# Optimization experiments

Measured on AMD Instinct MI355X. Metric: run time of the kernel, lower is better.

The kernel has to match this reference:

```python
import jax, jax.numpy as jnp
import numpy as np

DIM = 1024
HEADS = 16
HIDDEN = 4 * DIM

def _gelu_erf(x):
    # GELU via erf, matching the torch module exactly
    return x * 0.5 * (1.0 + jax.lax.erf(x / jnp.sqrt(2.0).astype(x.dtype)))

def setup_inputs() -> dict:
    key = jax.random.key(0)
    ks = jax.random.split(key, 12)
    s = 0.02
    x = jax.random.normal(ks[0], (2, 2048, DIM), dtype=jnp.float32)
    # MHSA params
    ln1_g = jnp.ones((DIM,), jnp.float32)
    ln1_b = jnp.zeros((DIM,), jnp.float32)
    w_qkv = jax.random.normal(ks[1], (DIM, 3 * DIM), jnp.float32) * s  # no bias
    w_proj = jax.random.normal(ks[2], (DIM, DIM), jnp.float32) * s
    b_proj = jnp.zeros((DIM,), jnp.float32)
    # ResMLP params
    ln2_g = jnp.ones((DIM,), jnp.float32)
    ln2_b = jnp.zeros((DIM,), jnp.float32)
    w1 = jax.random.normal(ks[3], (DIM, HIDDEN), jnp.float32) * s
    b1 = jnp.zeros((HIDDEN,), jnp.float32)
    w2 = jax.random.normal(ks[4], (HIDDEN, DIM), jnp.float32) * s
    b2 = jnp.zeros((DIM,), jnp.float32)
    return {"x": x, "ln1_g": ln1_g, "ln1_b": ln1_b, "w_qkv": w_qkv,
            "w_proj": w_proj, "b_proj": b_proj, "ln2_g": ln2_g, "ln2_b": ln2_b,
            "w1": w1, "b1": b1, "w2": w2, "b2": b2}

def _layernorm(x, g, b, eps=1e-5):
    mu = jnp.mean(x, axis=-1, keepdims=True)
    var = jnp.mean(jnp.square(x - mu), axis=-1, keepdims=True)
    return (x - mu) * jax.lax.rsqrt(var + eps) * g + b

def reference(x, ln1_g, ln1_b, w_qkv, w_proj, b_proj, ln2_g, ln2_b, w1, b1, w2, b2):
    B, N, C = x.shape
    H = HEADS
    hd = C // H
    scale = hd ** -0.5
    # --- MHSA (dropout is identity in eval) ---
    h = _layernorm(x, ln1_g, ln1_b)
    qkv = (h @ w_qkv).reshape(B, N, 3, H, hd)
    q = jnp.transpose(qkv[:, :, 0], (0, 2, 1, 3))  # [B,H,N,hd]
    k = jnp.transpose(qkv[:, :, 1], (0, 2, 1, 3))
    v = jnp.transpose(qkv[:, :, 2], (0, 2, 1, 3))
    attn = jax.nn.softmax(jnp.einsum('bhnd,bhmd->bhnm', q, k) * scale, axis=-1)
    out = jnp.einsum('bhnm,bhmd->bhnd', attn, v)
    out = jnp.transpose(out, (0, 2, 1, 3)).reshape(B, N, C)
    x = x + out @ w_proj + b_proj
    # --- ResMLP ---
    h = _layernorm(x, ln2_g, ln2_b)
    h = _gelu_erf(h @ w1 + b1)
    x = x + h @ w2 + b2
    return x
```

## Files before the change

kernel.cpp:

```cpp
#include <hip/hip_runtime.h>
#include <stdint.h>


#define DIMC 1024
#define HIDN 4096
#define SEQ  2048
#define TOK  4096

typedef __bf16 bf16x8 __attribute__((ext_vector_type(8)));
typedef float  f32x4  __attribute__((ext_vector_type(4)));
typedef unsigned short ushort8 __attribute__((ext_vector_type(8)));

__device__ inline unsigned short f2bf(float f) {
  union { float f; unsigned u; } v; v.f = f;
  unsigned u = v.u;
  return (unsigned short)((u + 0x7fffu + ((u >> 16) & 1u)) >> 16);
}

__device__ inline unsigned cvt_pk_bf16(float a, float b) {
  unsigned r;
  asm("v_cvt_pk_bf16_f32 %0, %1, %2" : "=v"(r) : "v"(a), "v"(b));
  return r;
}

#if __has_builtin(__builtin_amdgcn_exp2f)
__device__ inline float fast_exp2(float x) { return __builtin_amdgcn_exp2f(x); }
#else
__device__ inline float fast_exp2(float x) { return exp2f(x); }
#endif

__device__ inline f32x4 mfma_bf16(bf16x8 a, bf16x8 b, f32x4 c) {
  return __builtin_amdgcn_mfma_f32_16x16x32_bf16(a, b, c, 0, 0, 0);
}

typedef const __attribute__((address_space(1))) unsigned int* as1_u32p;
typedef __attribute__((address_space(3))) unsigned int* as3_u32p;
__device__ inline void gload_lds16(const unsigned short* g, unsigned short* l) {
  __builtin_amdgcn_global_load_lds((as1_u32p)(const void*)g, (as3_u32p)(void*)l,
                                   16, 0, 0);
}

__global__ __launch_bounds__(256)
void transpose_cast4(const float* __restrict__ wa, unsigned short* __restrict__ ta,
                     const float* __restrict__ wb, unsigned short* __restrict__ tb,
                     const float* __restrict__ wc, unsigned short* __restrict__ tc,
                     const float* __restrict__ wd, unsigned short* __restrict__ td) {
  __shared__ float tile[32][33];
  const int bid = blockIdx.x;
  const float* w; unsigned short* wt; int K, N, bx, by;
  if (bid < 3072)      { w = wa; wt = ta; K = 1024; N = 3072; bx = bid % 96;  by = bid / 96; }
  else if (bid < 4096) { int i = bid - 3072; w = wb; wt = tb; K = 1024; N = 1024; bx = i % 32;  by = i / 32; }
  else if (bid < 8192) { int i = bid - 4096; w = wc; wt = tc; K = 1024; N = 4096; bx = i % 128; by = i / 128; }
  else                 { int i = bid - 8192; w = wd; wt = td; K = 4096; N = 1024; bx = i % 32;  by = i / 32; }
  const int k0 = by * 32;
  const int n0 = bx * 32;
  const int tx = threadIdx.x & 31;
  const int ty = threadIdx.x >> 5;
#pragma unroll
  for (int i = 0; i < 4; i++)
    tile[ty + i * 8][tx] = w[(size_t)(k0 + ty + i * 8) * N + n0 + tx];
  __syncthreads();
#pragma unroll
  for (int i = 0; i < 4; i++)
    wt[(size_t)(n0 + ty + i * 8) * K + k0 + tx] = f2bf(tile[tx][ty + i * 8]);
}

__global__ __launch_bounds__(256)
void ln_kernel(const float* __restrict__ x, const float* __restrict__ g,
               const float* __restrict__ b, unsigned short* __restrict__ out) {
  const int row = blockIdx.x;
  const int tid = threadIdx.x;
  const float4* xr = (const float4*)&x[(size_t)row * DIMC];
  float4 v = xr[tid];
  float s  = v.x + v.y + v.z + v.w;
  float sq = v.x * v.x + v.y * v.y + v.z * v.z + v.w * v.w;
#pragma unroll
  for (int off = 32; off > 0; off >>= 1) {
    s  += __shfl_xor(s, off, 64);
    sq += __shfl_xor(sq, off, 64);
  }
  __shared__ float red[8];
  if ((tid & 63) == 0) { red[tid >> 6] = s; red[4 + (tid >> 6)] = sq; }
  __syncthreads();
  s  = red[0] + red[1] + red[2] + red[3];
  sq = red[4] + red[5] + red[6] + red[7];
  const float mu  = s * (1.0f / DIMC);
  const float var = sq * (1.0f / DIMC) - mu * mu;
  const float rs  = rsqrtf(var + 1e-5f);
  const int c = tid * 4;
  float vv[4] = {v.x, v.y, v.z, v.w};
#pragma unroll
  for (int j = 0; j < 4; j++)
    out[(size_t)row * DIMC + c + j] = f2bf((vv[j] - mu) * rs * g[c + j] + b[c + j]);
}

template <int EPI, int TN>
__global__ __launch_bounds__(256, (TN == 64) ? 4 : 3)
void gemm_bt(const unsigned short* __restrict__ A,
             const unsigned short* __restrict__ Bt,
             float* __restrict__ Cf, unsigned short* __restrict__ Cb,
             const float* __restrict__ bias, const float* __restrict__ res,
             int M, int N, int K,
             unsigned short* __restrict__ qd,
             unsigned short* __restrict__ kTd,
             unsigned short* __restrict__ vd) {
  constexpr int NU = TN / 32;
  constexpr int BP = TN / 32;
  __shared__ unsigned short As[128 * 64];
  __shared__ unsigned short Bs[TN * 64];
  const int gx  = N / TN;
  const int bid = blockIdx.x;
  const int xcd = bid & 7;
  const int lin = bid >> 3;
  const int bx  = lin % gx;
  const int by  = (xcd << 2) + lin / gx;
  const int tid  = threadIdx.x;
  const int lane = tid & 63;
  const int wave = tid >> 6;
  const int m0 = by * 128;
  const int n0 = bx * TN;
  const int wm = (wave >> 1) * 64;
  const int wn = (wave & 1) * (TN / 2);
  const int lm = lane & 15;
  const int lg = lane >> 4;
  const int r8 = tid >> 3;
  const int c8 = tid & 7;
  const int csrc = ((c8 ^ (r8 & 7)) * 8);

  const unsigned short* gA = &A [(size_t)(m0 + r8) * K + csrc];
  const unsigned short* gB = &Bt[(size_t)(n0 + r8) * K + csrc];

  f32x4 acc[4][NU];
#pragma unroll
  for (int t = 0; t < 4; t++)
#pragma unroll
    for (int u = 0; u < NU; u++) acc[t][u] = {0.f, 0.f, 0.f, 0.f};

  const int x0 = (lg ^ (lm & 7)) * 8;
  const int x1 = ((4 + lg) ^ (lm & 7)) * 8;

  for (int k0 = 0; k0 < K; k0 += 64) {
    __syncthreads();
#pragma unroll
    for (int p = 0; p < 4; p++)
      gload_lds16(gA + (size_t)p * 32 * K + k0, &As[p * 2048 + wave * 512]);
#pragma unroll
    for (int p = 0; p < BP; p++)
      gload_lds16(gB + (size_t)p * 32 * K + k0, &Bs[p * 2048 + wave * 512]);
    __syncthreads();
#pragma unroll
    for (int sub = 0; sub < 2; sub++) {
      const int xo = sub ? x1 : x0;
      bf16x8 af[4], bfr[NU];
#pragma unroll
      for (int t = 0; t < 4; t++)  af[t]  = *(const bf16x8*)&As[(wm + t * 16 + lm) * 64 + xo];
#pragma unroll
      for (int u = 0; u < NU; u++) bfr[u] = *(const bf16x8*)&Bs[(wn + u * 16 + lm) * 64 + xo];
#pragma unroll
      for (int t = 0; t < 4; t++)
#pragma unroll
        for (int u = 0; u < NU; u++)
          acc[t][u] = mfma_bf16(af[t], bfr[u], acc[t][u]);
    }
  }

#pragma unroll
  for (int t = 0; t < 4; t++) {
    const int row = m0 + wm + t * 16 + lg * 4;
#pragma unroll
    for (int u = 0; u < NU; u++) {
      const int col = n0 + wn + u * 16 + lm;
#pragma unroll
      for (int r = 0; r < 4; r++) {
        float v = acc[t][u][r];
        size_t idx = (size_t)(row + r) * N + col;
        if (EPI == 0) {
          const int rr = row + r;
          const int bb = rr >> 11, key = rr & (SEQ - 1);
          if (col < 1024) {
            qd[(size_t)rr * 1024 + col] = f2bf(v * 0.18033688011112042f);
          } else if (col < 2048) {
            const int d = col - 1024, h = d >> 6, dd = d & 63;
            kTd[(((size_t)(bb * 16 + h)) * SEQ + key) * 64 + dd] = f2bf(v);
          } else {
            vd[(size_t)rr * 1024 + (col - 2048)] = f2bf(v);
          }
        } else if (EPI == 1) {
          Cf[idx] = v + bias[col] + res[idx];
        } else {
          float xg = v + bias[col];
          Cb[idx] = f2bf(0.5f * xg * (1.0f + erff(xg * 0.70710678118654752f)));
        }
      }
    }
  }
}

__global__ __launch_bounds__(256)
void v_transpose(const unsigned short* __restrict__ vd,
                 unsigned short* __restrict__ vT) {
  const int kt = blockIdx.x;
  const int bh = blockIdx.y;
  const int b = bh >> 4, h = bh & 15;
  const int tid = threadIdx.x;
  __shared__ unsigned short tile[64 * 72];
  const int tok = tid >> 2;
  const int ch  = tid & 3;
  const size_t srow = (size_t)(b * SEQ + kt * 64 + tok) * 1024 + h * 64;
  ushort8 va = *(const ushort8*)&vd[srow + ch * 8];
  ushort8 vb = *(const ushort8*)&vd[srow + 32 + ch * 8];
  *(ushort8*)&tile[tok * 72 + ch * 8] = va;
  *(ushort8*)&tile[tok * 72 + 32 + ch * 8] = vb;
  __syncthreads();
  const int d = tid >> 2;
  ushort8 o0, o1;
#pragma unroll
  for (int j = 0; j < 8; j++) {
    o0[j] = tile[(ch * 8 + j) * 72 + d];
    o1[j] = tile[((ch + 4) * 8 + j) * 72 + d];
  }
  const size_t vdst = ((size_t)bh * 64 + d) * SEQ + kt * 64;
  *(ushort8*)&vT[vdst + ch * 8] = o0;
  *(ushort8*)&vT[vdst + 32 + ch * 8] = o1;
}

__global__ __launch_bounds__(256, 2)
void attn_kernel(const unsigned short* __restrict__ qbuf,
                 const unsigned short* __restrict__ kT,
                 const unsigned short* __restrict__ vT,
                 unsigned short* __restrict__ out) {
  const int bid = blockIdx.x;
  const int xcd = bid & 7;
  const int lin = bid >> 3;
  const int bh  = (xcd << 2) + (lin >> 4);
  const int qt  = lin & 15;
  const int b  = bh >> 4;
  const int h  = bh & 15;
  const int tid  = threadIdx.x;
  const int lane = tid & 63;
  const int wave = tid >> 6;
  const int ks   = wave >> 1;
  const int qh   = wave & 1;
  const int lm = lane & 15;
  const int lg = lane >> 4;

  __shared__ f32x4 shbuf[4096];
  unsigned short* Ks = (unsigned short*)shbuf;
  unsigned short* Vs = (unsigned short*)shbuf + 8192;
  unsigned short* Ps = (unsigned short*)shbuf + 16384;

  const int qrow_base = b * SEQ + qt * 128 + qh * 64;
  bf16x8 qb[4][2];
#pragma unroll
  for (int s = 0; s < 4; s++)
#pragma unroll
    for (int c = 0; c < 2; c++)
      qb[s][c] = *(const bf16x8*)&qbuf[(size_t)(qrow_base + s * 16 + lm) * 1024 +
                                       h * 64 + c * 32 + lg * 8];

  f32x4 o[4][4];
#pragma unroll
  for (int dt = 0; dt < 4; dt++)
#pragma unroll
    for (int s = 0; s < 4; s++) o[dt][s] = {0.f, 0.f, 0.f, 0.f};
  float li[4] = {0.f, 0.f, 0.f, 0.f};

  const unsigned short* kbp = &kT[(size_t)bh * SEQ * 64];
  const unsigned short* vbp = &vT[(size_t)bh * 64 * SEQ];
  const int ts   = tid & 127;
  const int srow = ts >> 3;
  const int slog = ((ts & 7) ^ (srow & 7)) * 8;
  const int koff = ks * 1024;
  const int xk0 = ((lg)     ^ (lm & 7)) * 8;
  const int xk1 = ((4 + lg) ^ (lm & 7)) * 8;
  unsigned short* ksb = Ks + ks * 4096;
  unsigned short* vsb = Vs + ks * 4096;
  unsigned short* psb = Ps + wave * 4096;
  unsigned short* kdst = ksb + ((ts >> 6) * 512);
  unsigned short* vdst = vsb + ((ts >> 6) * 512);

  for (int kt = 0; kt < 16; kt++) {
    __syncthreads();
#pragma unroll
    for (int p = 0; p < 4; p++) {
      gload_lds16(&kbp[(size_t)(koff + kt * 64 + p * 16 + srow) * 64 + slog],
                  kdst + p * 1024);
      gload_lds16(&vbp[(size_t)(p * 16 + srow) * SEQ + koff + kt * 64 + slog],
                  vdst + p * 1024);
    }
    __syncthreads();

#pragma unroll
    for (int u = 0; u < 4; u++) {
      bf16x8 ka0 = *(const bf16x8*)&ksb[(u * 16 + lm) * 64 + xk0];
      bf16x8 ka1 = *(const bf16x8*)&ksb[(u * 16 + lm) * 64 + xk1];
      f32x4 st[4];
#pragma unroll
      for (int s = 0; s < 4; s++) {
        f32x4 z = {0.f, 0.f, 0.f, 0.f};
        z = mfma_bf16(ka0, qb[s][0], z);
        z = mfma_bf16(ka1, qb[s][1], z);
        st[s] = z;
      }
#pragma unroll
      for (int s = 0; s < 4; s++) {
        float p0 = fast_exp2(st[s][0] - 8.0f);
        float p1 = fast_exp2(st[s][1] - 8.0f);
        float p2 = fast_exp2(st[s][2] - 8.0f);
        float p3 = fast_exp2(st[s][3] - 8.0f);
        li[s] += (p0 + p1) + (p2 + p3);
        uint2 pk;
        pk.x = cvt_pk_bf16(p0, p1);
        pk.y = cvt_pk_bf16(p2, p3);
        const int phys = (u * 2 + (lg >> 1)) ^ (lm & 7);
        *(uint2*)&psb[(s * 16 + lm) * 64 + phys * 8 + (lg & 1) * 4] = pk;
      }
    }

#pragma unroll
    for (int kc = 0; kc < 2; kc++) {
      const int xo = kc ? xk1 : xk0;
      bf16x8 pb[4];
#pragma unroll
      for (int s = 0; s < 4; s++)
        pb[s] = *(const bf16x8*)&psb[(s * 16 + lm) * 64 + xo];
#pragma unroll
      for (int dt = 0; dt < 4; dt++) {
        bf16x8 va = *(const bf16x8*)&vsb[(dt * 16 + lm) * 64 + xo];
#pragma unroll
        for (int s = 0; s < 4; s++)
          o[dt][s] = mfma_bf16(va, pb[s], o[dt][s]);
      }
    }
  }

  __syncthreads();
  f32x4* ob = shbuf + qh * 1088;
  float*  lb = (float*)(ob + 1024);
  if (ks == 1) {
#pragma unroll
    for (int dt = 0; dt < 4; dt++)
#pragma unroll
      for (int s = 0; s < 4; s++)
        ob[(dt * 4 + s) * 64 + lane] = o[dt][s];
#pragma unroll
    for (int s = 0; s < 4; s++) lb[s * 64 + lane] = li[s];
  }
  __syncthreads();
  if (ks == 0) {
#pragma unroll
    for (int dt = 0; dt < 4; dt++)
#pragma unroll
      for (int s = 0; s < 4; s++)
        o[dt][s] += ob[(dt * 4 + s) * 64 + lane];
#pragma unroll
    for (int s = 0; s < 4; s++) {
      float l = li[s] + lb[s * 64 + lane];
      l += __shfl_xor(l, 16, 64);
      l += __shfl_xor(l, 32, 64);
      const float inv = 1.0f / l;
#pragma unroll
      for (int dt = 0; dt < 4; dt++) {
        uint2 ok;
        ok.x = cvt_pk_bf16(o[dt][s][0] * inv, o[dt][s][1] * inv);
        ok.y = cvt_pk_bf16(o[dt][s][2] * inv, o[dt][s][3] * inv);
        *(uint2*)&out[(size_t)(qrow_base + s * 16 + lm) * DIMC + h * 64 +
                      dt * 16 + lg * 4] = ok;
      }
    }
  }
}

extern "C" void kernel_launch(void* const* d_in, const int* in_sizes, int n_in,
                              void* d_out, int out_size, void* d_ws, size_t ws_size,
                              hipStream_t stream) {
  const float* x      = (const float*)d_in[0];
  const float* ln1_g  = (const float*)d_in[1];
  const float* ln1_b  = (const float*)d_in[2];
  const float* w_qkv  = (const float*)d_in[3];
  const float* w_proj = (const float*)d_in[4];
  const float* b_proj = (const float*)d_in[5];
  const float* ln2_g  = (const float*)d_in[6];
  const float* ln2_b  = (const float*)d_in[7];
  const float* w1     = (const float*)d_in[8];
  const float* b1     = (const float*)d_in[9];
  const float* w2     = (const float*)d_in[10];
  const float* b2     = (const float*)d_in[11];
  float* out = (float*)d_out;

  char* ws = (char*)d_ws;
  size_t off = 0;
  auto alloc = [&](size_t bytes) { void* p = ws + off; off += (bytes + 255) & ~(size_t)255; return p; };
  unsigned short* wqkvT = (unsigned short*)alloc((size_t)3072 * 1024 * 2);
  unsigned short* wprjT = (unsigned short*)alloc((size_t)1024 * 1024 * 2);
  unsigned short* w1T   = (unsigned short*)alloc((size_t)4096 * 1024 * 2);
  unsigned short* w2T   = (unsigned short*)alloc((size_t)1024 * 4096 * 2);
  unsigned short* hb    = (unsigned short*)alloc((size_t)TOK * 1024 * 2);
  unsigned short* qbuf  = (unsigned short*)alloc((size_t)TOK * 1024 * 2);
  unsigned short* vdb   = (unsigned short*)alloc((size_t)TOK * 1024 * 2);
  unsigned short* attnb = (unsigned short*)alloc((size_t)TOK * 1024 * 2);
  float*          x1    = (float*)         alloc((size_t)TOK * 1024 * 4);
  unsigned short* hidb  = (unsigned short*)alloc((size_t)TOK * 4096 * 2);
  unsigned short* kT = hidb;
  unsigned short* vT = hidb + (size_t)32 * SEQ * 64;

  transpose_cast4<<<12288, 256, 0, stream>>>(w_qkv, wqkvT, w_proj, wprjT,
                                             w1, w1T, w2, w2T);
  ln_kernel<<<TOK, 256, 0, stream>>>(x, ln1_g, ln1_b, hb);
  gemm_bt<0, 128><<<768, 256, 0, stream>>>(
      hb, wqkvT, nullptr, nullptr, nullptr, nullptr, TOK, 3072, 1024,
      qbuf, kT, vdb);
  v_transpose<<<dim3(SEQ / 64, 32), 256, 0, stream>>>(vdb, vT);
  attn_kernel<<<512, 256, 0, stream>>>(qbuf, kT, vT, attnb);
  gemm_bt<1, 64><<<512, 256, 0, stream>>>(
      attnb, wprjT, x1, nullptr, b_proj, x, TOK, 1024, 1024,
      nullptr, nullptr, nullptr);
  ln_kernel<<<TOK, 256, 0, stream>>>(x1, ln2_g, ln2_b, hb);
  gemm_bt<2, 128><<<1024, 256, 0, stream>>>(
      hb, w1T, nullptr, hidb, b1, nullptr, TOK, 4096, 1024,
      nullptr, nullptr, nullptr);
  gemm_bt<1, 64><<<512, 256, 0, stream>>>(
      hidb, w2T, out, nullptr, b2, x1, TOK, 1024, 4096,
      nullptr, nullptr, nullptr);
}
```

Before: 342.9 us.

## Add 256x256 double-buffered 8-wave GEMM for QKV and MLP-up projections

Introduces a new 512-thread GEMM kernel with 256x256 output tiles, double-buffered LDS filled by direct global-to-LDS loads, XOR-swizzled LDS layout, and phased barriers with MFMA priority boosting. It also remaps blocks so that row tiles are grouped per XCD. The QKV and first MLP GEMMs are switched to this kernel to raise operand reuse per tile and overlap loads with MFMAs. In exchange it uses heavy register and LDS footprints and launches few blocks (192 and 256), which may leave compute units underused.

```diff
diff --git a/kernel.cpp b/kernel.cpp
--- a/kernel.cpp
+++ b/kernel.cpp
@@ -38,6 +38,13 @@
 __device__ inline void gload_lds16(const unsigned short* g, unsigned short* l) {
   __builtin_amdgcn_global_load_lds((as1_u32p)(const void*)g, (as3_u32p)(void*)l,
                                    16, 0, 0);
+}
+
+__device__ inline void phase_bar() {
+  asm volatile("" ::: "memory");
+  __builtin_amdgcn_s_barrier();
+  asm volatile("" ::: "memory");
+  __builtin_amdgcn_sched_barrier(0);
 }
 
 __global__ __launch_bounds__(256)
@@ -92,6 +99,181 @@
 #pragma unroll
   for (int j = 0; j < 4; j++)
     out[(size_t)row * DIMC + c + j] = f2bf((vv[j] - mu) * rs * g[c + j] + b[c + j]);
+}
+
+template <int EPI>
+__global__ __launch_bounds__(512, 2)
+void gemm256(const unsigned short* __restrict__ A,
+             const unsigned short* __restrict__ Bt,
+             unsigned short* __restrict__ Cb,
+             const float* __restrict__ bias,
+             int N, int K, int gx,
+             unsigned short* __restrict__ qd,
+             unsigned short* __restrict__ kTd,
+             unsigned short* __restrict__ vd) {
+  __shared__ unsigned short As[2][256 * 64];
+  __shared__ unsigned short Bs[2][256 * 64];
+  const int bid = blockIdx.x;
+  const int xcd = bid & 7;
+  const int lin = bid >> 3;
+  const int bx  = lin % gx;
+  const int by  = (xcd << 1) + lin / gx;
+  const int tid  = threadIdx.x;
+  const int lane = tid & 63;
+  const int wave = tid >> 6;
+  const int m0 = by * 256;
+  const int n0 = bx * 256;
+  const int wm = (wave >> 2) * 128;
+  const int wn = (wave & 3) * 64;
+  const int lm = lane & 15;
+  const int lg = lane >> 4;
+  const int r8 = tid >> 3;
+  const int c8 = tid & 7;
+  const int csrc = (c8 ^ (r8 & 7)) * 8;
+  const unsigned short* gA0 = &A [(size_t)(m0 + r8) * K + csrc];
+  const unsigned short* gB0 = &Bt[(size_t)(n0 + r8) * K + csrc];
+  const int ldsb = (wave * 8) * 64;
+  const int xo0 = ((lg)     ^ (lm & 7)) * 8;
+  const int xo1 = ((4 + lg) ^ (lm & 7)) * 8;
+  const int KT = K >> 6;
+
+  f32x4 acc[8][4];
+#pragma unroll
+  for (int i = 0; i < 8; i++)
+#pragma unroll
+    for (int j = 0; j < 4; j++) acc[i][j] = {0.f, 0.f, 0.f, 0.f};
+  bf16x8 areg[4][2];
+  bf16x8 breg[2][2][2];
+
+#pragma unroll
+  for (int q = 0; q < 4; ++q) {
+    gload_lds16(gA0 + (size_t)(q * 64) * K, &As[0][q * 4096 + ldsb]);
+    gload_lds16(gB0 + (size_t)(q * 64) * K, &Bs[0][q * 4096 + ldsb]);
+  }
+#pragma unroll
+  for (int q = 0; q < 4; ++q) {
+    gload_lds16(gA0 + (size_t)(q * 64) * K + 64, &As[1][q * 4096 + ldsb]);
+    gload_lds16(gB0 + (size_t)(q * 64) * K + 64, &Bs[1][q * 4096 + ldsb]);
+  }
+  asm volatile("s_waitcnt vmcnt(8)" ::: "memory");
+  phase_bar();
+
+  for (int kt = 0; kt < KT; ++kt) {
+    const int cur = kt & 1;
+    const unsigned short* Ac = As[cur];
+    const unsigned short* Bc = Bs[cur];
+    const int k2 = (kt + 2) << 6;
+    const bool more = (kt + 2) < KT;
+
+#pragma unroll
+    for (int mt = 0; mt < 4; ++mt) {
+      areg[mt][0] = *(const bf16x8*)&Ac[(wm + mt * 16 + lm) * 64 + xo0];
+      areg[mt][1] = *(const bf16x8*)&Ac[(wm + mt * 16 + lm) * 64 + xo1];
+    }
+#pragma unroll
+    for (int nt = 0; nt < 2; ++nt) {
+      breg[0][nt][0] = *(const bf16x8*)&Bc[(wn + nt * 16 + lm) * 64 + xo0];
+      breg[0][nt][1] = *(const bf16x8*)&Bc[(wn + nt * 16 + lm) * 64 + xo1];
+    }
+    phase_bar();
+    __builtin_amdgcn_s_setprio(1);
+#pragma unroll
+    for (int mt = 0; mt < 4; ++mt)
+#pragma unroll
+      for (int nt = 0; nt < 2; ++nt) {
+        acc[mt][nt] = mfma_bf16(areg[mt][0], breg[0][nt][0], acc[mt][nt]);
+        acc[mt][nt] = mfma_bf16(areg[mt][1], breg[0][nt][1], acc[mt][nt]);
+      }
+    __builtin_amdgcn_s_setprio(0);
+    phase_bar();
+
+#pragma unroll
+    for (int nt = 0; nt < 2; ++nt) {
+      breg[1][nt][0] = *(const bf16x8*)&Bc[(wn + (2 + nt) * 16 + lm) * 64 + xo0];
+      breg[1][nt][1] = *(const bf16x8*)&Bc[(wn + (2 + nt) * 16 + lm) * 64 + xo1];
+    }
+    phase_bar();
+    __builtin_amdgcn_s_setprio(1);
+#pragma unroll
+    for (int mt = 0; mt < 4; ++mt)
+#pragma unroll
+      for (int nt = 0; nt < 2; ++nt) {
+        acc[mt][2 + nt] = mfma_bf16(areg[mt][0], breg[1][nt][0], acc[mt][2 + nt]);
+        acc[mt][2 + nt] = mfma_bf16(areg[mt][1], breg[1][nt][1], acc[mt][2 + nt]);
+      }
+    __builtin_amdgcn_s_setprio(0);
+    phase_bar();
+
+#pragma unroll
+    for (int mt = 0; mt < 4; ++mt) {
+      areg[mt][0] = *(const bf16x8*)&Ac[(wm + (4 + mt) * 16 + lm) * 64 + xo0];
+      areg[mt][1] = *(const bf16x8*)&Ac[(wm + (4 + mt) * 16 + lm) * 64 + xo1];
+    }
+    if (more) {
+#pragma unroll
+      for (int q = 0; q < 4; ++q)
+        gload_lds16(gB0 + (size_t)(q * 64) * K + k2, &Bs[cur][q * 4096 + ldsb]);
+    }
+    phase_bar();
+    __builtin_amdgcn_s_setprio(1);
+#pragma unroll
+    for (int mt = 0; mt < 4; ++mt)
+#pragma unroll
+      for (int nt = 0; nt < 2; ++nt) {
+        acc[4 + mt][2 + nt] = mfma_bf16(areg[mt][0], breg[1][nt][0], acc[4 + mt][2 + nt]);
+        acc[4 + mt][2 + nt] = mfma_bf16(areg[mt][1], breg[1][nt][1], acc[4 + mt][2 + nt]);
+      }
+    __builtin_amdgcn_s_setprio(0);
+    phase_bar();
+
+    if (more) {
+#pragma unroll
+      for (int q = 0; q < 4; ++q)
+        gload_lds16(gA0 + (size_t)(q * 64) * K + k2, &As[cur][q * 4096 + ldsb]);
+    }
+    phase_bar();
+    __builtin_amdgcn_s_setprio(1);
+#pragma unroll
+    for (int mt = 0; mt < 4; ++mt)
+#pragma unroll
+      for (int nt = 0; nt < 2; ++nt) {
+        acc[4 + mt][nt] = mfma_bf16(areg[mt][0], breg[0][nt][0], acc[4 + mt][nt]);
+        acc[4 + mt][nt] = mfma_bf16(areg[mt][1], breg[0][nt][1], acc[4 + mt][nt]);
+      }
+    __builtin_amdgcn_s_setprio(0);
+    if (more)                asm volatile("s_waitcnt vmcnt(8)" ::: "memory");
+    else if (kt + 1 < KT)    asm volatile("s_waitcnt vmcnt(0)" ::: "memory");
+    phase_bar();
+  }
+
+#pragma unroll
+  for (int mt = 0; mt < 8; ++mt) {
+    const int row = m0 + wm + mt * 16 + lg * 4;
+#pragma unroll
+    for (int nt = 0; nt < 4; ++nt) {
+      const int col = n0 + wn + nt * 16 + lm;
+#pragma unroll
+      for (int r = 0; r < 4; ++r) {
+        float v = acc[mt][nt][r];
+        if (EPI == 0) {
+          const int rr = row + r;
+          const int bb = rr >> 11, key = rr & (SEQ - 1);
+          if (col < 1024) {
+            qd[(size_t)rr * 1024 + col] = f2bf(v * 0.18033688011112042f);
+          } else if (col < 2048) {
+            const int d = col - 1024, h = d >> 6, dd = d & 63;
+            kTd[(((size_t)(bb * 16 + h)) * SEQ + key) * 64 + dd] = f2bf(v);
+          } else {
+            vd[(size_t)(row + r) * 1024 + (col - 2048)] = f2bf(v);
+          }
+        } else {
+          float xg = v + bias[col];
+          Cb[(size_t)(row + r) * N + col] =
+              f2bf(0.5f * xg * (1.0f + erff(xg * 0.70710678118654752f)));
+        }
+      }
+    }
+  }
 }
 
 template <int EPI, int TN>
@@ -174,18 +356,7 @@
       for (int r = 0; r < 4; r++) {
         float v = acc[t][u][r];
         size_t idx = (size_t)(row + r) * N + col;
-        if (EPI == 0) {
-          const int rr = row + r;
-          const int bb = rr >> 11, key = rr & (SEQ - 1);
-          if (col < 1024) {
-            qd[(size_t)rr * 1024 + col] = f2bf(v * 0.18033688011112042f);
-          } else if (col < 2048) {
-            const int d = col - 1024, h = d >> 6, dd = d & 63;
-            kTd[(((size_t)(bb * 16 + h)) * SEQ + key) * 64 + dd] = f2bf(v);
-          } else {
-            vd[(size_t)rr * 1024 + (col - 2048)] = f2bf(v);
-          }
-        } else if (EPI == 1) {
+        if (EPI == 1) {
           Cf[idx] = v + bias[col] + res[idx];
         } else {
           float xg = v + bias[col];
@@ -407,18 +578,16 @@
   transpose_cast4<<<12288, 256, 0, stream>>>(w_qkv, wqkvT, w_proj, wprjT,
                                              w1, w1T, w2, w2T);
   ln_kernel<<<TOK, 256, 0, stream>>>(x, ln1_g, ln1_b, hb);
-  gemm_bt<0, 128><<<768, 256, 0, stream>>>(
-      hb, wqkvT, nullptr, nullptr, nullptr, nullptr, TOK, 3072, 1024,
-      qbuf, kT, vdb);
+  gemm256<0><<<192, 512, 0, stream>>>(
+      hb, wqkvT, nullptr, nullptr, 3072, 1024, 12, qbuf, kT, vdb);
   v_transpose<<<dim3(SEQ / 64, 32), 256, 0, stream>>>(vdb, vT);
   attn_kernel<<<512, 256, 0, stream>>>(qbuf, kT, vT, attnb);
   gemm_bt<1, 64><<<512, 256, 0, stream>>>(
       attnb, wprjT, x1, nullptr, b_proj, x, TOK, 1024, 1024,
       nullptr, nullptr, nullptr);
   ln_kernel<<<TOK, 256, 0, stream>>>(x1, ln2_g, ln2_b, hb);
-  gemm_bt<2, 128><<<1024, 256, 0, stream>>>(
-      hb, w1T, nullptr, hidb, b1, nullptr, TOK, 4096, 1024,
-      nullptr, nullptr, nullptr);
+  gemm256<2><<<256, 512, 0, stream>>>(
+      hb, w1T, hidb, b1, 4096, 1024, 16, nullptr, nullptr, nullptr);
   gemm_bt<1, 64><<<512, 256, 0, stream>>>(
       hidb, w2T, out, nullptr, b2, x1, TOK, 1024, 4096,
       nullptr, nullptr, nullptr);
```

New measurement: 351.2 us. 1.02x slower.

## Add 256x256 double-buffered GEMM kernel for QKV and MLP-up projections

Applied to the files above, without the earlier changes.

Introduces a new 512-thread GEMM with 256x256 output tiles, double-buffered LDS staging via direct global-to-LDS loads, XOR-swizzled layout, and a hand-scheduled barrier/priority sequence interleaving MFMA with prefetch. It replaces the 128-wide gemm_bt for the QKV projection and the GELU MLP-up projection, aiming for more data reuse per loaded tile and better overlap of loads with matrix math. The larger tiles launch fewer blocks (192 and 256 over 256 CUs), which risks poor occupancy and load imbalance, and raises register pressure.

```diff
diff --git a/kernel.cpp b/kernel.cpp
--- a/kernel.cpp
+++ b/kernel.cpp
@@ -38,6 +38,19 @@
 __device__ inline void gload_lds16(const unsigned short* g, unsigned short* l) {
   __builtin_amdgcn_global_load_lds((as1_u32p)(const void*)g, (as3_u32p)(void*)l,
                                    16, 0, 0);
+}
+
+__device__ inline void bar_mid() {
+  asm volatile("" ::: "memory");
+  __builtin_amdgcn_s_barrier();
+  asm volatile("s_waitcnt lgkmcnt(0)" ::: "memory");
+  __builtin_amdgcn_sched_barrier(0);
+}
+__device__ inline void bar_end() {
+  asm volatile("" ::: "memory");
+  __builtin_amdgcn_s_barrier();
+  asm volatile("" ::: "memory");
+  __builtin_amdgcn_sched_barrier(0);
 }
 
 __global__ __launch_bounds__(256)
@@ -94,16 +107,159 @@
     out[(size_t)row * DIMC + c + j] = f2bf((vv[j] - mu) * rs * g[c + j] + b[c + j]);
 }
 
+template <int EPI, int N, int K, int GX>
+__global__ __launch_bounds__(512, 2)
+void gemm256(const unsigned short* __restrict__ A,
+             const unsigned short* __restrict__ Bt,
+             unsigned short* __restrict__ Cb,
+             const float* __restrict__ bias,
+             unsigned short* __restrict__ qd,
+             unsigned short* __restrict__ kTd,
+             unsigned short* __restrict__ vd) {
+  constexpr int KT = K >> 6;
+  static_assert((KT & 1) == 0 && KT >= 4, "KT must be even, >=4");
+  __shared__ unsigned short As0[256 * 64];
+  __shared__ unsigned short Bs0[256 * 64];
+  __shared__ unsigned short As1[256 * 64];
+  __shared__ unsigned short Bs1[256 * 64];
+  const int bid = blockIdx.x;
+  const int xcd = bid & 7;
+  const int lin = bid >> 3;
+  const int bx  = lin % GX;
+  const int by  = (xcd << 1) + lin / GX;
+  const int tid  = threadIdx.x;
+  const int lane = tid & 63;
+  const int wave = tid >> 6;
+  const int m0 = by * 256;
+  const int n0 = bx * 256;
+  const int wm = (wave >> 2) * 128;
+  const int wn = (wave & 3) * 64;
+  const int lm = lane & 15;
+  const int lg = lane >> 4;
+  const int r8 = tid >> 3;
+  const int c8 = tid & 7;
+  const int csrc = (c8 ^ (r8 & 7)) * 8;
+  const unsigned short* gA0 = &A [(size_t)(m0 + r8) * K + csrc];
+  const unsigned short* gB0 = &Bt[(size_t)(n0 + r8) * K + csrc];
+  const int ldsb = wave * 512;
+  const int xo0 = ((lg)     ^ (lm & 7)) * 8;
+  const int xo1 = ((4 + lg) ^ (lm & 7)) * 8;
+
+  f32x4 acc[8][4];
+#pragma unroll
+  for (int i = 0; i < 8; i++)
+#pragma unroll
+    for (int j = 0; j < 4; j++) acc[i][j] = {0.f, 0.f, 0.f, 0.f};
+  bf16x8 af[4][2];
+  bf16x8 b0r[2][2];
+  bf16x8 b1r[2][2];
+
+  auto LDA = [&](const unsigned short* buf, const int mh) {
+#pragma unroll
+    for (int mt = 0; mt < 4; ++mt) {
+      const int row = wm + mh * 64 + mt * 16 + lm;
+      af[mt][0] = *(const bf16x8*)&buf[row * 64 + xo0];
+      af[mt][1] = *(const bf16x8*)&buf[row * 64 + xo1];
+    }
+  };
+  auto LDB = [&](const unsigned short* buf, const int nh, bf16x8 (&br)[2][2]) {
+#pragma unroll
+    for (int nt = 0; nt < 2; ++nt) {
+      const int row = wn + nh * 32 + nt * 16 + lm;
+      br[nt][0] = *(const bf16x8*)&buf[row * 64 + xo0];
+      br[nt][1] = *(const bf16x8*)&buf[row * 64 + xo1];
+    }
+  };
+  auto MM = [&](const int mh, const int nh, bf16x8 (&br)[2][2]) {
+    __builtin_amdgcn_s_setprio(1);
+#pragma unroll
+    for (int mt = 0; mt < 4; ++mt)
+#pragma unroll
+      for (int nt = 0; nt < 2; ++nt) {
+        acc[mh * 4 + mt][nh * 2 + nt] =
+            mfma_bf16(af[mt][0], br[nt][0], acc[mh * 4 + mt][nh * 2 + nt]);
+        acc[mh * 4 + mt][nh * 2 + nt] =
+            mfma_bf16(af[mt][1], br[nt][1], acc[mh * 4 + mt][nh * 2 + nt]);
+      }
+    __builtin_amdgcn_s_setprio(0);
+  };
+  auto STGA = [&](unsigned short* buf, const int kt) {
+#pragma unroll
+    for (int q = 0; q < 4; ++q)
+      gload_lds16(gA0 + (size_t)(q * 64) * K + kt * 64, &buf[q * 4096 + ldsb]);
+  };
+  auto STGB = [&](unsigned short* buf, const int kt) {
+#pragma unroll
+    for (int q = 0; q < 4; ++q)
+      gload_lds16(gB0 + (size_t)(q * 64) * K + kt * 64, &buf[q * 4096 + ldsb]);
+  };
+  auto QUAD = [&](const unsigned short* AS, const unsigned short* BS,
+                  unsigned short* sA, unsigned short* sB, const int skt,
+                  const int wmode) {
+    LDA(AS, 0); LDB(BS, 0, b0r);
+    bar_mid(); MM(0, 0, b0r); bar_end();
+    LDB(BS, 1, b1r);
+    bar_mid(); MM(0, 1, b1r); bar_end();
+    LDA(AS, 1);
+    if (skt >= 0) STGB(sB, skt);
+    bar_mid(); MM(1, 1, b1r); bar_end();
+    if (skt >= 0) STGA(sA, skt);
+    bar_mid(); MM(1, 0, b0r);
+    if (wmode == 8)      asm volatile("s_waitcnt vmcnt(8)" ::: "memory");
+    else if (wmode == 0) asm volatile("s_waitcnt vmcnt(0)" ::: "memory");
+    bar_end();
+  };
+
+  STGA(As0, 0); STGB(Bs0, 0);
+  STGA(As1, 1); STGB(Bs1, 1);
+  asm volatile("s_waitcnt vmcnt(8)" ::: "memory");
+  bar_end();
+
+#pragma unroll 1
+  for (int i = 0; i < KT / 2 - 1; ++i) {
+    QUAD(As0, Bs0, As0, Bs0, 2 * i + 2, 8);
+    QUAD(As1, Bs1, As1, Bs1, 2 * i + 3, 8);
+  }
+  QUAD(As0, Bs0, nullptr, nullptr, -1, 0);
+  QUAD(As1, Bs1, nullptr, nullptr, -1, -1);
+
+#pragma unroll
+  for (int mt = 0; mt < 8; ++mt) {
+    const int row = m0 + wm + mt * 16 + lg * 4;
+#pragma unroll
+    for (int nt = 0; nt < 4; ++nt) {
+      const int col = n0 + wn + nt * 16 + lm;
+#pragma unroll
+      for (int r = 0; r < 4; ++r) {
+        float v = acc[mt][nt][r];
+        if (EPI == 0) {
+          const int rr = row + r;
+          const int bb = rr >> 11, key = rr & (SEQ - 1);
+          if (col < 1024) {
+            qd[(size_t)rr * 1024 + col] = f2bf(v * 0.18033688011112042f);
+          } else if (col < 2048) {
+            const int d = col - 1024, h = d >> 6, dd = d & 63;
+            kTd[(((size_t)(bb * 16 + h)) * SEQ + key) * 64 + dd] = f2bf(v);
+          } else {
+            vd[(size_t)(row + r) * 1024 + (col - 2048)] = f2bf(v);
+          }
+        } else {
+          float xg = v + bias[col];
+          Cb[(size_t)(row + r) * N + col] =
+              f2bf(0.5f * xg * (1.0f + erff(xg * 0.70710678118654752f)));
+        }
+      }
+    }
+  }
+}
+
 template <int EPI, int TN>
 __global__ __launch_bounds__(256, (TN == 64) ? 4 : 3)
 void gemm_bt(const unsigned short* __restrict__ A,
              const unsigned short* __restrict__ Bt,
              float* __restrict__ Cf, unsigned short* __restrict__ Cb,
              const float* __restrict__ bias, const float* __restrict__ res,
-             int M, int N, int K,
-             unsigned short* __restrict__ qd,
-             unsigned short* __restrict__ kTd,
-             unsigned short* __restrict__ vd) {
+             int M, int N, int K) {
   constexpr int NU = TN / 32;
   constexpr int BP = TN / 32;
   __shared__ unsigned short As[128 * 64];
@@ -174,18 +330,7 @@
       for (int r = 0; r < 4; r++) {
         float v = acc[t][u][r];
         size_t idx = (size_t)(row + r) * N + col;
-        if (EPI == 0) {
-          const int rr = row + r;
-          const int bb = rr >> 11, key = rr & (SEQ - 1);
-          if (col < 1024) {
-            qd[(size_t)rr * 1024 + col] = f2bf(v * 0.18033688011112042f);
-          } else if (col < 2048) {
-            const int d = col - 1024, h = d >> 6, dd = d & 63;
-            kTd[(((size_t)(bb * 16 + h)) * SEQ + key) * 64 + dd] = f2bf(v);
-          } else {
-            vd[(size_t)rr * 1024 + (col - 2048)] = f2bf(v);
-          }
-        } else if (EPI == 1) {
+        if (EPI == 1) {
           Cf[idx] = v + bias[col] + res[idx];
         } else {
           float xg = v + bias[col];
@@ -407,19 +552,15 @@
   transpose_cast4<<<12288, 256, 0, stream>>>(w_qkv, wqkvT, w_proj, wprjT,
                                              w1, w1T, w2, w2T);
   ln_kernel<<<TOK, 256, 0, stream>>>(x, ln1_g, ln1_b, hb);
-  gemm_bt<0, 128><<<768, 256, 0, stream>>>(
-      hb, wqkvT, nullptr, nullptr, nullptr, nullptr, TOK, 3072, 1024,
-      qbuf, kT, vdb);
+  gemm256<0, 3072, 1024, 12><<<192, 512, 0, stream>>>(
+      hb, wqkvT, nullptr, nullptr, qbuf, kT, vdb);
   v_transpose<<<dim3(SEQ / 64, 32), 256, 0, stream>>>(vdb, vT);
   attn_kernel<<<512, 256, 0, stream>>>(qbuf, kT, vT, attnb);
   gemm_bt<1, 64><<<512, 256, 0, stream>>>(
-      attnb, wprjT, x1, nullptr, b_proj, x, TOK, 1024, 1024,
-      nullptr, nullptr, nullptr);
+      attnb, wprjT, x1, nullptr, b_proj, x, TOK, 1024, 1024);
   ln_kernel<<<TOK, 256, 0, stream>>>(x1, ln2_g, ln2_b, hb);
-  gemm_bt<2, 128><<<1024, 256, 0, stream>>>(
-      hb, w1T, nullptr, hidb, b1, nullptr, TOK, 4096, 1024,
-      nullptr, nullptr, nullptr);
+  gemm256<2, 4096, 1024, 16><<<256, 512, 0, stream>>>(
+      hb, w1T, hidb, b1, nullptr, nullptr, nullptr);
   gemm_bt<1, 64><<<512, 256, 0, stream>>>(
-      hidb, w2T, out, nullptr, b2, x1, TOK, 1024, 4096,
-      nullptr, nullptr, nullptr);
-}
+      hidb, w2T, out, nullptr, b2, x1, TOK, 1024, 4096);
+}
```

Result: no change. 347.1 us (+1.2%).
